# Kernel tuning notes

Measured on AMD Instinct MI355X. Metric: run time of the kernel, lower is better.

The kernel has to match this reference:

```python
import jax, jax.numpy as jnp
import numpy as np

EPS = 1e-5


def cheb_conv(x, edge, W, b):
    # x: [B, N, C], edge: [2, E], W: [3, C, F], b: [F]
    # PyG ChebConv, K=3, normalized Laplacian, lambda_max=2 -> L_hat = -D^-1/2 A D^-1/2
    row, col = edge[0], edge[1]
    N = x.shape[1]
    deg = jnp.zeros((N,), x.dtype).at[row].add(1.0)
    dis = jnp.where(deg > 0, 1.0 / jnp.sqrt(jnp.maximum(deg, 1.0)), 0.0)
    we = (-dis[row] * dis[col])[None, :, None]  # [1, E, 1]
    prop = lambda z: jnp.zeros_like(z).at[:, row].add(z[:, col] * we)
    Tx0 = x
    Tx1 = prop(Tx0)
    Tx2 = 2.0 * prop(Tx1) - Tx0
    out = (jnp.einsum('bnc,cf->bnf', Tx0, W[0])
           + jnp.einsum('bnc,cf->bnf', Tx1, W[1])
           + jnp.einsum('bnc,cf->bnf', Tx2, W[2]))
    return out + b


def lbr(x, W, b, g, be):
    # Linear -> BatchNorm1d (batch stats) -> ReLU (dropout prob = 0)
    h = x @ W + b
    h = (h - h.mean(0)) / jnp.sqrt(h.var(0) + EPS) * g + be
    return jax.nn.relu(h)


def setup_inputs() -> dict:
    key = jax.random.key(0)
    ks = jax.random.split(key, 32)
    B, H = 32, 32
    Ns = [16384, 4096, 1024, 128]
    Es = [131072, 32768, 8192, 1024]
    F = Ns[3] * H  # 4096 flattened dim
    L = 128
    d = {}
    d['x'] = jax.random.normal(ks[0], (B, Ns[0], 3), jnp.float32)
    for i in range(4):
        d[f'e{i}'] = jax.random.randint(ks[1 + i], (2, Es[i]), 0, Ns[i])
    for i in range(3):
        d[f'l{i}'] = jnp.sort(jax.random.randint(ks[5 + i], (Ns[i + 1],), 0, Ns[i]))
    s = 0.1
    d['Wc1'] = jax.random.normal(ks[8], (3, 3, H), jnp.float32) * s
    d['b1'] = jnp.zeros((H,), jnp.float32)
    for i, nm in enumerate(['Wc2', 'Wc3', 'Wc4', 'Wc5']):
        d[nm] = jax.random.normal(ks[9 + i], (3, H, H), jnp.float32) * s
        d['b' + str(i + 2)] = jnp.zeros((H,), jnp.float32)
    sf = 1.0 / np.sqrt(F).astype(np.float32)
    for i, nm in enumerate(['W6', 'W7', 'W8']):
        d[nm] = jax.random.normal(ks[13 + i], (F, F), jnp.float32) * sf
        d['b' + str(i + 6)] = jnp.zeros((F,), jnp.float32)
        d['g' + str(i + 6)] = jnp.ones((F,), jnp.float32)
        d['be' + str(i + 6)] = jnp.zeros((F,), jnp.float32)
    d['W9'] = jax.random.normal(ks[16], (F, L), jnp.float32) * sf
    d['b9'] = jnp.zeros((L,), jnp.float32)
    return d


def reference(x, Wc1, b1, Wc2, b2, Wc3, b3, Wc4, b4, Wc5, b5,
              W6, b6, g6, be6, W7, b7, g7, be7, W8, b8, g8, be8, W9, b9,
              e0, e1, e2, e3, l0, l1, l2):
    x = cheb_conv(x, e0, Wc1, b1)                       # level 0
    x = jnp.tanh(cheb_conv(x[:, l0], e1, Wc2, b2))      # CTP: pool -> Cheb -> tanh
    x = jnp.tanh(cheb_conv(x[:, l1], e2, Wc3, b3))
    x = jnp.tanh(cheb_conv(x[:, l2], e3, Wc4, b4))
    x = cheb_conv(x, e3, Wc5, b5)                       # level 3, [B, N3, H]
    x = x.reshape(x.shape[0], -1)                       # [B, N3*H]
    x = lbr(lbr(lbr(x, W6, b6, g6, be6), W7, b7, g7, be7), W8, b8, g8, be8)
    mu = x @ W9 + b9
    mu = (mu - mu.mean(0)) / jnp.sqrt(mu.var(0) + EPS)  # BatchNorm1d affine=False
    return mu
```

## Files before the change

### kernel.cpp

```cpp
#include <hip/hip_runtime.h>
#include <hip/hip_bf16.h>

#define BB 32
#define HD 32
#define N0 16384
#define C0 3
#define E0v 131072
#define N1 4096
#define E1v 32768
#define N2 1024
#define E2v 8192
#define N3 128
#define E3v 1024
#define FDIM 4096
#define LDIM 128
#define NT (N0 + N1 + N2 + N3)
#define ET (E0v + E1v + E2v + E3v)
#define EPSBN 1e-5f
#define KC 64

__global__ void k_count(const int* __restrict__ e0, const int* __restrict__ e1,
                        const int* __restrict__ e2, const int* __restrict__ e3,
                        int* __restrict__ deg) {
    int e = blockIdx.x * 256 + threadIdx.x;
    if (e >= ET) return;
    const int* p; int idx, nb;
    if (e < E0v)                     { p = e0; idx = e; nb = 0; }
    else if (e < E0v + E1v)          { p = e1; idx = e - E0v; nb = N0; }
    else if (e < E0v + E1v + E2v)    { p = e2; idx = e - E0v - E1v; nb = N0 + N1; }
    else                             { p = e3; idx = e - E0v - E1v - E2v; nb = N0 + N1 + N2; }
    atomicAdd(&deg[nb + p[idx]], 1);
}

__global__ void __launch_bounds__(1024) k_scan(const int* __restrict__ deg,
                                               int* __restrict__ offs, int* __restrict__ cur) {
    __shared__ int ss[1024];
    int t = threadIdx.x, base = t * 22;
    int loc[22]; int s = 0;
#pragma unroll
    for (int i = 0; i < 22; i++) {
        int idx = base + i;
        int v = (idx < NT) ? deg[idx] : 0;
        loc[i] = s; s += v;
    }
    ss[t] = s;
    __syncthreads();
    int run = s;
    for (int o = 1; o < 1024; o <<= 1) {
        int y = (t >= o) ? ss[t - o] : 0;
        __syncthreads();
        run += y; ss[t] = run;
        __syncthreads();
    }
    int excl = run - s;
#pragma unroll
    for (int i = 0; i < 22; i++) {
        int idx = base + i;
        if (idx < NT) { int v = excl + loc[i]; offs[idx] = v; cur[idx] = v; }
    }
    if (t == 0) offs[NT] = ET;
}

__global__ void k_scatter(const int* __restrict__ e0, const int* __restrict__ e1,
                          const int* __restrict__ e2, const int* __restrict__ e3,
                          const int* __restrict__ deg, int* __restrict__ cur,
                          int* __restrict__ ccol, float* __restrict__ cw) {
    int e = blockIdx.x * 256 + threadIdx.x;
    if (e >= ET) return;
    const int* p; int idx, nb, El;
    if (e < E0v)                  { p = e0; idx = e; nb = 0; El = E0v; }
    else if (e < E0v + E1v)       { p = e1; idx = e - E0v; nb = N0; El = E1v; }
    else if (e < E0v + E1v + E2v) { p = e2; idx = e - E0v - E1v; nb = N0 + N1; El = E2v; }
    else                          { p = e3; idx = e - E0v - E1v - E2v; nb = N0 + N1 + N2; El = E3v; }
    int r = p[idx], c = p[El + idx];
    int pos = atomicAdd(&cur[nb + r], 1);
    int dr = deg[nb + r], dc = deg[nb + c];
    float w = 0.f;
    if (dr > 0 && dc > 0)
        w = -(1.f / sqrtf((float)dr)) * (1.f / sqrtf((float)dc));
    ccol[pos] = c;
    cw[pos] = w;
}

__global__ void k_transpose(const float* __restrict__ x, float* __restrict__ xt) {
    __shared__ float t0[32][33], t1[32][33], t2[32][33];
    int tx = threadIdx.x, ty = threadIdx.y;
    int n0 = blockIdx.x * 32;
#pragma unroll
    for (int i = 0; i < 4; i++) {
        int b = ty * 4 + i;
        size_t base = ((size_t)b * N0 + n0 + tx) * 3;
        t0[tx][b] = x[base];
        t1[tx][b] = x[base + 1];
        t2[tx][b] = x[base + 2];
    }
    __syncthreads();
#pragma unroll
    for (int i = 0; i < 4; i++) {
        int nl = ty * 4 + i;
        size_t o = (size_t)(n0 + nl) * 96 + tx * 3;
        xt[o]     = t0[nl][tx];
        xt[o + 1] = t1[nl][tx];
        xt[o + 2] = t2[nl][tx];
    }
}

__global__ void k_prop0(const float* __restrict__ xt, float* __restrict__ T1t,
                        const int* __restrict__ offs, const int* __restrict__ ccol,
                        const float* __restrict__ cw) {
    int idx = blockIdx.x * 256 + threadIdx.x;
    int n = (unsigned)idx / 96u;
    int q = idx - n * 96;
    int s = offs[n], e = offs[n + 1];
    float acc = 0.f;
    for (int k = s; k < e; k++)
        acc += cw[k] * xt[(size_t)ccol[k] * 96 + q];
    T1t[idx] = acc;
}

__global__ void k_comb0(const float* __restrict__ xt, const float* __restrict__ T1t,
                        const int* __restrict__ offs, const int* __restrict__ ccol,
                        const float* __restrict__ cw, const int* __restrict__ pool,
                        const float* __restrict__ W, const float* __restrict__ bias,
                        float* __restrict__ Yout) {
    __shared__ float s0[96], s1[96], s2[96], sw[288], sb[32];
    int t = threadIdx.x;
    int j = blockIdx.x;
    int n = pool[j];
    size_t nb = (size_t)n * 96;
    s0[t] = xt[nb + t];
    s1[t] = T1t[nb + t];
    if (t < 32) { s0[64 + t] = xt[nb + 64 + t]; s1[64 + t] = T1t[nb + 64 + t]; }
    {
        int s = offs[n], e = offs[n + 1];
        float a0 = 0.f, a1 = 0.f;
        for (int k = s; k < e; k++) {
            const float* bp = T1t + (size_t)ccol[k] * 96;
            float w = cw[k];
            a0 += w * bp[t];
            if (t < 32) a1 += w * bp[64 + t];
        }
        s2[t] = a0;
        if (t < 32) s2[64 + t] = a1;
    }
    for (int i = t; i < 288; i += 64) sw[i] = W[i];
    if (t < 32) sb[t] = bias[t];
    __syncthreads();

    int f0 = (t & 7) * 4;
    int b0 = (t >> 3) * 4;
    float acc[4][4];
#pragma unroll
    for (int bi = 0; bi < 4; bi++)
#pragma unroll
        for (int fi = 0; fi < 4; fi++) acc[bi][fi] = sb[f0 + fi];
#pragma unroll
    for (int c = 0; c < 3; c++) {
        float4 w0 = *(float4*)&sw[(0 * 3 + c) * 32 + f0];
        float4 w1 = *(float4*)&sw[(1 * 3 + c) * 32 + f0];
        float4 w2 = *(float4*)&sw[(2 * 3 + c) * 32 + f0];
#pragma unroll
        for (int bi = 0; bi < 4; bi++) {
            int b = b0 + bi;
            float x0 = s0[b * 3 + c], x1 = s1[b * 3 + c];
            float x2 = 2.f * s2[b * 3 + c] - x0;
            acc[bi][0] += x0 * w0.x + x1 * w1.x + x2 * w2.x;
            acc[bi][1] += x0 * w0.y + x1 * w1.y + x2 * w2.y;
            acc[bi][2] += x0 * w0.z + x1 * w1.z + x2 * w2.z;
            acc[bi][3] += x0 * w0.w + x1 * w1.w + x2 * w2.w;
        }
    }
#pragma unroll
    for (int bi = 0; bi < 4; bi++) {
        float4 v = { acc[bi][0], acc[bi][1], acc[bi][2], acc[bi][3] };
        *(float4*)&Yout[(size_t)j * 1024 + (b0 + bi) * 32 + f0] = v;
    }
}

__global__ void k_propC(const float* __restrict__ Yin, float* __restrict__ T1,
                        const int* __restrict__ offs, const int* __restrict__ ccol,
                        const float* __restrict__ cw) {
    int idx = blockIdx.x * 256 + threadIdx.x;
    int n = idx >> 10;
    int q = idx & 1023;
    int s = offs[n], e = offs[n + 1];
    float acc = 0.f;
    for (int k = s; k < e; k++)
        acc += cw[k] * Yin[((size_t)ccol[k] << 10) + q];
    T1[idx] = acc;
}

__global__ void k_combC(const float* __restrict__ Yin, const float* __restrict__ T1,
                        const int* __restrict__ offs, const int* __restrict__ ccol,
                        const float* __restrict__ cw, const int* __restrict__ pool,
                        const float* __restrict__ W, const float* __restrict__ bias,
                        float* __restrict__ Yout, int doTanh, int bMajor) {
    __shared__ float s0[32 * 33], s1[32 * 33], s2[32 * 33], sw[3072], sb[32];
    int t = threadIdx.x;
    int j = blockIdx.x;
    int n = pool ? pool[j] : j;
    size_t nb = (size_t)n << 10;
#pragma unroll
    for (int i = 0; i < 16; i++) {
        int q = t + i * 64;
        int li = (q >> 5) * 33 + (q & 31);
        s0[li] = Yin[nb + q];
        s1[li] = T1[nb + q];
    }
    {
        int s = offs[n], e = offs[n + 1];
        float ga[16];
#pragma unroll
        for (int i = 0; i < 16; i++) ga[i] = 0.f;
        for (int k = s; k < e; k++) {
            const float* bp = T1 + ((size_t)ccol[k] << 10);
            float w = cw[k];
#pragma unroll
            for (int i = 0; i < 16; i++) ga[i] += w * bp[t + i * 64];
        }
#pragma unroll
        for (int i = 0; i < 16; i++) {
            int q = t + i * 64;
            s2[(q >> 5) * 33 + (q & 31)] = ga[i];
        }
    }
    for (int i = t; i < 768; i += 64) ((float4*)sw)[i] = ((const float4*)W)[i];
    if (t < 32) sb[t] = bias[t];
    __syncthreads();

    int f0 = (t & 7) * 4;
    int b0 = (t >> 3) * 4;
    float acc[4][4];
#pragma unroll
    for (int bi = 0; bi < 4; bi++)
#pragma unroll
        for (int fi = 0; fi < 4; fi++) acc[bi][fi] = sb[f0 + fi];
    for (int c = 0; c < 32; c++) {
        float4 w0 = *(float4*)&sw[c * 32 + f0];
        float4 w1 = *(float4*)&sw[1024 + c * 32 + f0];
        float4 w2 = *(float4*)&sw[2048 + c * 32 + f0];
#pragma unroll
        for (int bi = 0; bi < 4; bi++) {
            int li = (b0 + bi) * 33 + c;
            float x0 = s0[li], x1 = s1[li];
            float x2 = 2.f * s2[li] - x0;
            acc[bi][0] += x0 * w0.x + x1 * w1.x + x2 * w2.x;
            acc[bi][1] += x0 * w0.y + x1 * w1.y + x2 * w2.y;
            acc[bi][2] += x0 * w0.z + x1 * w1.z + x2 * w2.z;
            acc[bi][3] += x0 * w0.w + x1 * w1.w + x2 * w2.w;
        }
    }
    if (doTanh) {
#pragma unroll
        for (int bi = 0; bi < 4; bi++)
#pragma unroll
            for (int fi = 0; fi < 4; fi++) acc[bi][fi] = tanhf(acc[bi][fi]);
    }
#pragma unroll
    for (int bi = 0; bi < 4; bi++) {
        float4 v = { acc[bi][0], acc[bi][1], acc[bi][2], acc[bi][3] };
        if (bMajor)
            *(float4*)&Yout[(size_t)(b0 + bi) * FDIM + j * 32 + f0] = v;
        else
            *(float4*)&Yout[((size_t)j << 10) + (b0 + bi) * 32 + f0] = v;
    }
}

__global__ void __launch_bounds__(256, 2) k_gemm(const float* __restrict__ Z,
                                                 const float* __restrict__ W,
                                                 float* __restrict__ Hp) {
    int t = threadIdx.x; int bx = blockIdx.x; int kc = blockIdx.y; int kb = kc * 64;
    __shared__ float zs[32][64];
    for (int i = t; i < 512; i += 256) {
        int fl = i * 4; int b = fl >> 6; int k = fl & 63;
        *(float4*)&zs[b][k] = *(const float4*)&Z[(size_t)b * 4096 + kb + k];
    }
    __syncthreads();
    int ft = t & 63, bt = t >> 6;
    int f0 = bx * 256 + ft * 4;
    int b0 = bt * 8;
    const float* Wp = W + (size_t)kb * 4096 + f0;
    float acc[8][4];
#pragma unroll
    for (int bi = 0; bi < 8; bi++)
#pragma unroll
        for (int fi = 0; fi < 4; fi++) acc[bi][fi] = 0.f;
    for (int k4 = 0; k4 < 16; k4++) {
        float4 w[4];
#pragma unroll
        for (int j = 0; j < 4; j++)
            w[j] = *(const float4*)&Wp[(size_t)(k4 * 4 + j) * 4096];
        float4 z[8];
#pragma unroll
        for (int bi = 0; bi < 8; bi++)
            z[bi] = *(const float4*)&zs[b0 + bi][k4 * 4];
#pragma unroll
        for (int bi = 0; bi < 8; bi++) {
            acc[bi][0] += z[bi].x * w[0].x + z[bi].y * w[1].x + z[bi].z * w[2].x + z[bi].w * w[3].x;
            acc[bi][1] += z[bi].x * w[0].y + z[bi].y * w[1].y + z[bi].z * w[2].y + z[bi].w * w[3].y;
            acc[bi][2] += z[bi].x * w[0].z + z[bi].y * w[1].z + z[bi].z * w[2].z + z[bi].w * w[3].z;
            acc[bi][3] += z[bi].x * w[0].w + z[bi].y * w[1].w + z[bi].z * w[2].w + z[bi].w * w[3].w;
        }
    }
    float* o = Hp + (size_t)kc * 32 * 4096;
#pragma unroll
    for (int bi = 0; bi < 8; bi++) {
        float4 v = { acc[bi][0], acc[bi][1], acc[bi][2], acc[bi][3] };
        *(float4*)&o[(size_t)(b0 + bi) * 4096 + f0] = v;
    }
}

__global__ void k_bnrelu(const float* __restrict__ Hp, const float* __restrict__ g,
                         const float* __restrict__ be, float* __restrict__ Zo) {
    __shared__ float sA[8][33], sB[8][33], sm[32], si[32];
    int t = threadIdx.x; int fq = t & 31; int bq = t >> 5;
    int f = blockIdx.x * 32 + fq;
    float v[4];
#pragma unroll
    for (int i = 0; i < 4; i++) v[i] = 0.f;
    for (int p = 0; p < KC; p++) {
        const float* hp = Hp + (size_t)p * 32 * 4096;
#pragma unroll
        for (int i = 0; i < 4; i++) v[i] += hp[(size_t)(bq * 4 + i) * 4096 + f];
    }
    float a = 0.f, q = 0.f;
#pragma unroll
    for (int i = 0; i < 4; i++) { a += v[i]; q += v[i] * v[i]; }
    sA[bq][fq] = a; sB[bq][fq] = q;
    __syncthreads();
    if (t < 32) {
        float m = 0.f, qq = 0.f;
#pragma unroll
        for (int i = 0; i < 8; i++) { m += sA[i][t]; qq += sB[i][t]; }
        m *= (1.f / 32.f);
        qq = qq * (1.f / 32.f) - m * m;
        sm[t] = m; si[t] = rsqrtf(fmaxf(qq, 0.f) + EPSBN);
    }
    __syncthreads();
    float m = sm[fq], inv = si[fq], gg = g[f], bb = be[f];
#pragma unroll
    for (int i = 0; i < 4; i++) {
        float o = (v[i] - m) * inv * gg + bb;
        Zo[(size_t)(bq * 4 + i) * 4096 + f] = fmaxf(o, 0.f);
    }
}

__global__ void __launch_bounds__(128, 2) k_gemm9(const float* __restrict__ Z,
                                                  const float* __restrict__ W9,
                                                  float* __restrict__ Mp) {
    int t = threadIdx.x; int kc = blockIdx.x; int kb = kc * 64;
    __shared__ float zs[32][64];
    for (int i = t; i < 512; i += 128) {
        int fl = i * 4; int b = fl >> 6; int k = fl & 63;
        *(float4*)&zs[b][k] = *(const float4*)&Z[(size_t)b * 4096 + kb + k];
    }
    __syncthreads();
    int ft = t & 31, bt = t >> 5;
    int f0 = ft * 4;
    int b0 = bt * 8;
    const float* Wp = W9 + (size_t)kb * 128 + f0;
    float acc[8][4];
#pragma unroll
    for (int bi = 0; bi < 8; bi++)
#pragma unroll
        for (int fi = 0; fi < 4; fi++) acc[bi][fi] = 0.f;
    for (int k4 = 0; k4 < 16; k4++) {
        float4 w[4];
#pragma unroll
        for (int j = 0; j < 4; j++)
            w[j] = *(const float4*)&Wp[(size_t)(k4 * 4 + j) * 128];
        float4 z[8];
#pragma unroll
        for (int bi = 0; bi < 8; bi++)
            z[bi] = *(const float4*)&zs[b0 + bi][k4 * 4];
#pragma unroll
        for (int bi = 0; bi < 8; bi++) {
            acc[bi][0] += z[bi].x * w[0].x + z[bi].y * w[1].x + z[bi].z * w[2].x + z[bi].w * w[3].x;
            acc[bi][1] += z[bi].x * w[0].y + z[bi].y * w[1].y + z[bi].z * w[2].y + z[bi].w * w[3].y;
            acc[bi][2] += z[bi].x * w[0].z + z[bi].y * w[1].z + z[bi].z * w[2].z + z[bi].w * w[3].z;
            acc[bi][3] += z[bi].x * w[0].w + z[bi].y * w[1].w + z[bi].z * w[2].w + z[bi].w * w[3].w;
        }
    }
    float* o = Mp + (size_t)kc * 32 * 128;
#pragma unroll
    for (int bi = 0; bi < 8; bi++) {
        float4 v = { acc[bi][0], acc[bi][1], acc[bi][2], acc[bi][3] };
        *(float4*)&o[(b0 + bi) * 128 + f0] = v;
    }
}

__global__ void k_red9(const float* __restrict__ Mp, float* __restrict__ Mu) {
    int idx = blockIdx.x * 256 + threadIdx.x;
    if (idx >= 4096) return;
    float a = 0.f;
    for (int p = 0; p < KC; p++) a += Mp[(size_t)p * 4096 + idx];
    Mu[idx] = a;
}

__global__ void k_bnfinal(const float* __restrict__ Mu, float* __restrict__ out) {
    int f = threadIdx.x;
    float v[32], s = 0.f;
#pragma unroll
    for (int b = 0; b < 32; b++) { v[b] = Mu[b * 128 + f]; s += v[b]; }
    float m = s * (1.f / 32.f), q = 0.f;
#pragma unroll
    for (int b = 0; b < 32; b++) { float d = v[b] - m; q += d * d; }
    float inv = rsqrtf(q * (1.f / 32.f) + EPSBN);
#pragma unroll
    for (int b = 0; b < 32; b++) out[b * 128 + f] = (v[b] - m) * inv;
}

extern "C" void kernel_launch(void* const* d_in, const int* in_sizes, int n_in,
                              void* d_out, int out_size, void* d_ws, size_t ws_size,
                              hipStream_t stream) {
    const float* x  = (const float*)d_in[0];
    const int* e0 = (const int*)d_in[1];
    const int* e1 = (const int*)d_in[2];
    const int* e2 = (const int*)d_in[3];
    const int* e3 = (const int*)d_in[4];
    const int* l0 = (const int*)d_in[5];
    const int* l1 = (const int*)d_in[6];
    const int* l2 = (const int*)d_in[7];
    const float* Wc1 = (const float*)d_in[8];
    const float* b1  = (const float*)d_in[9];
    const float* Wc2 = (const float*)d_in[10];
    const float* b2  = (const float*)d_in[11];
    const float* Wc3 = (const float*)d_in[12];
    const float* b3  = (const float*)d_in[13];
    const float* Wc4 = (const float*)d_in[14];
    const float* b4  = (const float*)d_in[15];
    const float* Wc5 = (const float*)d_in[16];
    const float* b5  = (const float*)d_in[17];
    const float* W6  = (const float*)d_in[18];
    const float* g6  = (const float*)d_in[20];
    const float* be6 = (const float*)d_in[21];
    const float* W7  = (const float*)d_in[22];
    const float* g7  = (const float*)d_in[24];
    const float* be7 = (const float*)d_in[25];
    const float* W8  = (const float*)d_in[26];
    const float* g8  = (const float*)d_in[28];
    const float* be8 = (const float*)d_in[29];
    const float* W9  = (const float*)d_in[30];
    float* out = (float*)d_out;

    char* p = (char*)d_ws;
    size_t o = 0;
    auto carve = [&](size_t bytes) {
        void* r = (void*)(p + o);
        o += (bytes + 255) & ~(size_t)255;
        return r;
    };
    float* xt  = (float*)carve((size_t)N0 * 96 * 4);
    float* T1t = (float*)carve((size_t)N0 * 96 * 4);
    float* Y1  = (float*)carve((size_t)N1 * 1024 * 4);
    float* T1c = (float*)carve((size_t)N1 * 1024 * 4);
    float* Y2  = (float*)carve((size_t)N2 * 1024 * 4);
    float* Y3  = (float*)carve((size_t)N3 * 1024 * 4);
    float* Y4  = (float*)carve((size_t)N3 * 1024 * 4);
    float* Zb0 = (float*)carve((size_t)BB * FDIM * 4);
    float* Zb1 = (float*)carve((size_t)BB * FDIM * 4);
    float* Mp  = (float*)carve((size_t)KC * BB * LDIM * 4);
    float* Mu  = (float*)carve((size_t)BB * LDIM * 4);
    int* deg  = (int*)carve(NT * sizeof(int));
    int* offs = (int*)carve((NT + 1) * sizeof(int));
    int* cur  = (int*)carve(NT * sizeof(int));
    int* ccol = (int*)carve(ET * sizeof(int));
    float* cw = (float*)carve(ET * sizeof(float));
    float* Hp = xt;
    (void)ws_size;

    hipMemsetAsync(deg, 0, NT * sizeof(int), stream);
    k_count<<<(ET + 255) / 256, 256, 0, stream>>>(e0, e1, e2, e3, deg);
    k_scan<<<1, 1024, 0, stream>>>(deg, offs, cur);
    k_scatter<<<(ET + 255) / 256, 256, 0, stream>>>(e0, e1, e2, e3, deg, cur, ccol, cw);

    const int* off0 = offs;
    const int* off1 = offs + N0;
    const int* off2 = offs + N0 + N1;
    const int* off3 = offs + N0 + N1 + N2;

    k_transpose<<<N0 / 32, dim3(32, 8), 0, stream>>>(x, xt);

    k_prop0<<<(N0 * 96) / 256, 256, 0, stream>>>(xt, T1t, off0, ccol, cw);
    k_comb0<<<N1, 64, 0, stream>>>(xt, T1t, off0, ccol, cw, l0, Wc1, b1, Y1);
    k_propC<<<(N1 * 1024) / 256, 256, 0, stream>>>(Y1, T1c, off1, ccol, cw);
    k_combC<<<N2, 64, 0, stream>>>(Y1, T1c, off1, ccol, cw, l1, Wc2, b2, Y2, 1, 0);
    k_propC<<<(N2 * 1024) / 256, 256, 0, stream>>>(Y2, T1c, off2, ccol, cw);
    k_combC<<<N3, 64, 0, stream>>>(Y2, T1c, off2, ccol, cw, l2, Wc3, b3, Y3, 1, 0);
    k_propC<<<(N3 * 1024) / 256, 256, 0, stream>>>(Y3, T1c, off3, ccol, cw);
    k_combC<<<N3, 64, 0, stream>>>(Y3, T1c, off3, ccol, cw, nullptr, Wc4, b4, Y4, 1, 0);
    k_propC<<<(N3 * 1024) / 256, 256, 0, stream>>>(Y4, T1c, off3, ccol, cw);
    k_combC<<<N3, 64, 0, stream>>>(Y4, T1c, off3, ccol, cw, nullptr, Wc5, b5, Zb0, 0, 1);

    const float* Ws[3]  = { W6, W7, W8 };
    const float* gs[3]  = { g6, g7, g8 };
    const float* bes[3] = { be6, be7, be8 };
    float* zin = Zb0; float* zout = Zb1;
    for (int l = 0; l < 3; l++) {
        k_gemm<<<dim3(16, KC), 256, 0, stream>>>(zin, Ws[l], Hp);
        k_bnrelu<<<128, 256, 0, stream>>>(Hp, gs[l], bes[l], zout);
        float* tmp = zin; zin = zout; zout = tmp;
    }
    k_gemm9<<<KC, 128, 0, stream>>>(zin, W9, Mp);
    k_red9<<<16, 256, 0, stream>>>(Mp, Mu);
    k_bnfinal<<<1, 128, 0, stream>>>(Mu, out);
    (void)out_size; (void)n_in; (void)in_sizes;
}
```

Before: 533.6 us.

## Pack CSR edges, vectorize gathers with float4, and reduce GEMM split-K partials

Stores each CSR edge's column and weight together as an int2 so the gathers issue one load per edge. The propagation and combine kernels now gather float4 vectors, and propC runs one block per node. The dense GEMM's split-K factor drops from 64 to 16, with each block looping over four 64-wide K sub-chunks, which shrinks the partial-sum buffer written and then re-reduced by the BN kernel. The risk is fewer GEMM blocks, which may underfill the GPU while streaming the weights.

Measured after the change: 553.1 us. +3.7%, slower.

```diff
diff --git a/kernel.cpp b/kernel.cpp
--- a/kernel.cpp
+++ b/kernel.cpp
@@ -17,7 +17,8 @@
 #define NT (N0 + N1 + N2 + N3)
 #define ET (E0v + E1v + E2v + E3v)
 #define EPSBN 1e-5f
-#define KC 64
+#define KC 16
+#define KC9 64
 
 __global__ void k_count(const int* __restrict__ e0, const int* __restrict__ e1,
                         const int* __restrict__ e2, const int* __restrict__ e3,
@@ -64,7 +65,7 @@
 __global__ void k_scatter(const int* __restrict__ e0, const int* __restrict__ e1,
                           const int* __restrict__ e2, const int* __restrict__ e3,
                           const int* __restrict__ deg, int* __restrict__ cur,
-                          int* __restrict__ ccol, float* __restrict__ cw) {
+                          int2* __restrict__ cpk) {
     int e = blockIdx.x * 256 + threadIdx.x;
     if (e >= ET) return;
     const int* p; int idx, nb, El;
@@ -78,8 +79,7 @@
     float w = 0.f;
     if (dr > 0 && dc > 0)
         w = -(1.f / sqrtf((float)dr)) * (1.f / sqrtf((float)dc));
-    ccol[pos] = c;
-    cw[pos] = w;
+    cpk[pos] = make_int2(c, __float_as_int(w));
 }
 
 __global__ void k_transpose(const float* __restrict__ x, float* __restrict__ xt) {
@@ -106,42 +106,44 @@
 }
 
 __global__ void k_prop0(const float* __restrict__ xt, float* __restrict__ T1t,
-                        const int* __restrict__ offs, const int* __restrict__ ccol,
-                        const float* __restrict__ cw) {
+                        const int* __restrict__ offs, const int2* __restrict__ cpk) {
     int idx = blockIdx.x * 256 + threadIdx.x;
-    int n = (unsigned)idx / 96u;
-    int q = idx - n * 96;
+    int n = (unsigned)idx / 24u;
+    int q = (idx - n * 24) * 4;
     int s = offs[n], e = offs[n + 1];
-    float acc = 0.f;
-    for (int k = s; k < e; k++)
-        acc += cw[k] * xt[(size_t)ccol[k] * 96 + q];
-    T1t[idx] = acc;
+    float4 acc = { 0.f, 0.f, 0.f, 0.f };
+    for (int k = s; k < e; k++) {
+        int2 ew = cpk[k];
+        float w = __int_as_float(ew.y);
+        float4 v = *(const float4*)&xt[(size_t)ew.x * 96 + q];
+        acc.x += w * v.x; acc.y += w * v.y; acc.z += w * v.z; acc.w += w * v.w;
+    }
+    *(float4*)&T1t[(size_t)n * 96 + q] = acc;
 }
 
 __global__ void k_comb0(const float* __restrict__ xt, const float* __restrict__ T1t,
-                        const int* __restrict__ offs, const int* __restrict__ ccol,
-                        const float* __restrict__ cw, const int* __restrict__ pool,
+                        const int* __restrict__ offs, const int2* __restrict__ cpk,
+                        const int* __restrict__ pool,
                         const float* __restrict__ W, const float* __restrict__ bias,
                         float* __restrict__ Yout) {
-    __shared__ float s0[96], s1[96], s2[96], sw[288], sb[32];
+    __shared__ __align__(16) float s0[96], s1[96], s2[96];
+    __shared__ float sw[288], sb[32];
     int t = threadIdx.x;
     int j = blockIdx.x;
     int n = pool[j];
     size_t nb = (size_t)n * 96;
-    s0[t] = xt[nb + t];
-    s1[t] = T1t[nb + t];
-    if (t < 32) { s0[64 + t] = xt[nb + 64 + t]; s1[64 + t] = T1t[nb + 64 + t]; }
-    {
+    if (t < 24) {
+        *(float4*)&s0[t * 4] = *(const float4*)&xt[nb + t * 4];
+        *(float4*)&s1[t * 4] = *(const float4*)&T1t[nb + t * 4];
         int s = offs[n], e = offs[n + 1];
-        float a0 = 0.f, a1 = 0.f;
+        float4 ga = { 0.f, 0.f, 0.f, 0.f };
         for (int k = s; k < e; k++) {
-            const float* bp = T1t + (size_t)ccol[k] * 96;
-            float w = cw[k];
-            a0 += w * bp[t];
-            if (t < 32) a1 += w * bp[64 + t];
-        }
-        s2[t] = a0;
-        if (t < 32) s2[64 + t] = a1;
+            int2 ew = cpk[k];
+            float w = __int_as_float(ew.y);
+            float4 v = *(const float4*)&T1t[(size_t)ew.x * 96 + t * 4];
+            ga.x += w * v.x; ga.y += w * v.y; ga.z += w * v.z; ga.w += w * v.w;
+        }
+        *(float4*)&s2[t * 4] = ga;
     }
     for (int i = t; i < 288; i += 64) sw[i] = W[i];
     if (t < 32) sb[t] = bias[t];
@@ -178,21 +180,23 @@
 }
 
 __global__ void k_propC(const float* __restrict__ Yin, float* __restrict__ T1,
-                        const int* __restrict__ offs, const int* __restrict__ ccol,
-                        const float* __restrict__ cw) {
-    int idx = blockIdx.x * 256 + threadIdx.x;
-    int n = idx >> 10;
-    int q = idx & 1023;
+                        const int* __restrict__ offs, const int2* __restrict__ cpk) {
+    int n = blockIdx.x;
+    int q = threadIdx.x * 4;
     int s = offs[n], e = offs[n + 1];
-    float acc = 0.f;
-    for (int k = s; k < e; k++)
-        acc += cw[k] * Yin[((size_t)ccol[k] << 10) + q];
-    T1[idx] = acc;
+    float4 acc = { 0.f, 0.f, 0.f, 0.f };
+    for (int k = s; k < e; k++) {
+        int2 ew = cpk[k];
+        float w = __int_as_float(ew.y);
+        float4 v = *(const float4*)&Yin[((size_t)ew.x << 10) + q];
+        acc.x += w * v.x; acc.y += w * v.y; acc.z += w * v.z; acc.w += w * v.w;
+    }
+    *(float4*)&T1[((size_t)n << 10) + q] = acc;
 }
 
 __global__ void k_combC(const float* __restrict__ Yin, const float* __restrict__ T1,
-                        const int* __restrict__ offs, const int* __restrict__ ccol,
-                        const float* __restrict__ cw, const int* __restrict__ pool,
+                        const int* __restrict__ offs, const int2* __restrict__ cpk,
+                        const int* __restrict__ pool,
                         const float* __restrict__ W, const float* __restrict__ bias,
                         float* __restrict__ Yout, int doTanh, int bMajor) {
     __shared__ float s0[32 * 33], s1[32 * 33], s2[32 * 33], sw[3072], sb[32];
@@ -201,27 +205,35 @@
     int n = pool ? pool[j] : j;
     size_t nb = (size_t)n << 10;
 #pragma unroll
-    for (int i = 0; i < 16; i++) {
-        int q = t + i * 64;
+    for (int i = 0; i < 4; i++) {
+        int q = t * 4 + i * 256;
+        float4 v0 = *(const float4*)&Yin[nb + q];
+        float4 v1 = *(const float4*)&T1[nb + q];
         int li = (q >> 5) * 33 + (q & 31);
-        s0[li] = Yin[nb + q];
-        s1[li] = T1[nb + q];
+        s0[li] = v0.x; s0[li + 1] = v0.y; s0[li + 2] = v0.z; s0[li + 3] = v0.w;
+        s1[li] = v1.x; s1[li + 1] = v1.y; s1[li + 2] = v1.z; s1[li + 3] = v1.w;
     }
     {
         int s = offs[n], e = offs[n + 1];
-        float ga[16];
-#pragma unroll
-        for (int i = 0; i < 16; i++) ga[i] = 0.f;
+        float4 ga[4];
+#pragma unroll
+        for (int i = 0; i < 4; i++) ga[i] = make_float4(0.f, 0.f, 0.f, 0.f);
         for (int k = s; k < e; k++) {
-            const float* bp = T1 + ((size_t)ccol[k] << 10);
-            float w = cw[k];
-#pragma unroll
-            for (int i = 0; i < 16; i++) ga[i] += w * bp[t + i * 64];
-        }
-#pragma unroll
-        for (int i = 0; i < 16; i++) {
-            int q = t + i * 64;
-            s2[(q >> 5) * 33 + (q & 31)] = ga[i];
+            int2 ew = cpk[k];
+            float w = __int_as_float(ew.y);
+            const float* bp = T1 + ((size_t)ew.x << 10);
+#pragma unroll
+            for (int i = 0; i < 4; i++) {
+                float4 v = *(const float4*)&bp[t * 4 + i * 256];
+                ga[i].x += w * v.x; ga[i].y += w * v.y;
+                ga[i].z += w * v.z; ga[i].w += w * v.w;
+            }
+        }
+#pragma unroll
+        for (int i = 0; i < 4; i++) {
+            int q = t * 4 + i * 256;
+            int li = (q >> 5) * 33 + (q & 31);
+            s2[li] = ga[i].x; s2[li + 1] = ga[i].y; s2[li + 2] = ga[i].z; s2[li + 3] = ga[i].w;
         }
     }
     for (int i = t; i < 768; i += 64) ((float4*)sw)[i] = ((const float4*)W)[i];
@@ -269,37 +281,41 @@
 __global__ void __launch_bounds__(256, 2) k_gemm(const float* __restrict__ Z,
                                                  const float* __restrict__ W,
                                                  float* __restrict__ Hp) {
-    int t = threadIdx.x; int bx = blockIdx.x; int kc = blockIdx.y; int kb = kc * 64;
+    int t = threadIdx.x; int bx = blockIdx.x; int kc = blockIdx.y;
     __shared__ float zs[32][64];
-    for (int i = t; i < 512; i += 256) {
-        int fl = i * 4; int b = fl >> 6; int k = fl & 63;
-        *(float4*)&zs[b][k] = *(const float4*)&Z[(size_t)b * 4096 + kb + k];
-    }
-    __syncthreads();
     int ft = t & 63, bt = t >> 6;
     int f0 = bx * 256 + ft * 4;
     int b0 = bt * 8;
-    const float* Wp = W + (size_t)kb * 4096 + f0;
     float acc[8][4];
 #pragma unroll
     for (int bi = 0; bi < 8; bi++)
 #pragma unroll
         for (int fi = 0; fi < 4; fi++) acc[bi][fi] = 0.f;
-    for (int k4 = 0; k4 < 16; k4++) {
-        float4 w[4];
-#pragma unroll
-        for (int j = 0; j < 4; j++)
-            w[j] = *(const float4*)&Wp[(size_t)(k4 * 4 + j) * 4096];
-        float4 z[8];
-#pragma unroll
-        for (int bi = 0; bi < 8; bi++)
-            z[bi] = *(const float4*)&zs[b0 + bi][k4 * 4];
-#pragma unroll
-        for (int bi = 0; bi < 8; bi++) {
-            acc[bi][0] += z[bi].x * w[0].x + z[bi].y * w[1].x + z[bi].z * w[2].x + z[bi].w * w[3].x;
-            acc[bi][1] += z[bi].x * w[0].y + z[bi].y * w[1].y + z[bi].z * w[2].y + z[bi].w * w[3].y;
-            acc[bi][2] += z[bi].x * w[0].z + z[bi].y * w[1].z + z[bi].z * w[2].z + z[bi].w * w[3].z;
-            acc[bi][3] += z[bi].x * w[0].w + z[bi].y * w[1].w + z[bi].z * w[2].w + z[bi].w * w[3].w;
+    for (int sc = 0; sc < 4; sc++) {
+        int kb = kc * 256 + sc * 64;
+        __syncthreads();
+        for (int i = t; i < 512; i += 256) {
+            int fl = i * 4; int b = fl >> 6; int k = fl & 63;
+            *(float4*)&zs[b][k] = *(const float4*)&Z[(size_t)b * 4096 + kb + k];
+        }
+        __syncthreads();
+        const float* Wp = W + (size_t)kb * 4096 + f0;
+        for (int k4 = 0; k4 < 16; k4++) {
+            float4 w[4];
+#pragma unroll
+            for (int j = 0; j < 4; j++)
+                w[j] = *(const float4*)&Wp[(size_t)(k4 * 4 + j) * 4096];
+            float4 z[8];
+#pragma unroll
+            for (int bi = 0; bi < 8; bi++)
+                z[bi] = *(const float4*)&zs[b0 + bi][k4 * 4];
+#pragma unroll
+            for (int bi = 0; bi < 8; bi++) {
+                acc[bi][0] += z[bi].x * w[0].x + z[bi].y * w[1].x + z[bi].z * w[2].x + z[bi].w * w[3].x;
+                acc[bi][1] += z[bi].x * w[0].y + z[bi].y * w[1].y + z[bi].z * w[2].y + z[bi].w * w[3].y;
+                acc[bi][2] += z[bi].x * w[0].z + z[bi].y * w[1].z + z[bi].z * w[2].z + z[bi].w * w[3].z;
+                acc[bi][3] += z[bi].x * w[0].w + z[bi].y * w[1].w + z[bi].z * w[2].w + z[bi].w * w[3].w;
+            }
         }
     }
     float* o = Hp + (size_t)kc * 32 * 4096;
@@ -393,7 +409,7 @@
     int idx = blockIdx.x * 256 + threadIdx.x;
     if (idx >= 4096) return;
     float a = 0.f;
-    for (int p = 0; p < KC; p++) a += Mp[(size_t)p * 4096 + idx];
+    for (int p = 0; p < KC9; p++) a += Mp[(size_t)p * 4096 + idx];
     Mu[idx] = a;
 }
 
@@ -459,20 +475,19 @@
     float* Y4  = (float*)carve((size_t)N3 * 1024 * 4);
     float* Zb0 = (float*)carve((size_t)BB * FDIM * 4);
     float* Zb1 = (float*)carve((size_t)BB * FDIM * 4);
-    float* Mp  = (float*)carve((size_t)KC * BB * LDIM * 4);
+    float* Mp  = (float*)carve((size_t)KC9 * BB * LDIM * 4);
     float* Mu  = (float*)carve((size_t)BB * LDIM * 4);
     int* deg  = (int*)carve(NT * sizeof(int));
     int* offs = (int*)carve((NT + 1) * sizeof(int));
     int* cur  = (int*)carve(NT * sizeof(int));
-    int* ccol = (int*)carve(ET * sizeof(int));
-    float* cw = (float*)carve(ET * sizeof(float));
+    int2* cpk = (int2*)carve(ET * sizeof(int2));
     float* Hp = xt;
     (void)ws_size;
 
     hipMemsetAsync(deg, 0, NT * sizeof(int), stream);
     k_count<<<(ET + 255) / 256, 256, 0, stream>>>(e0, e1, e2, e3, deg);
     k_scan<<<1, 1024, 0, stream>>>(deg, offs, cur);
-    k_scatter<<<(ET + 255) / 256, 256, 0, stream>>>(e0, e1, e2, e3, deg, cur, ccol, cw);
+    k_scatter<<<(ET + 255) / 256, 256, 0, stream>>>(e0, e1, e2, e3, deg, cur, cpk);
 
     const int* off0 = offs;
     const int* off1 = offs + N0;
@@ -481,16 +496,16 @@
 
     k_transpose<<<N0 / 32, dim3(32, 8), 0, stream>>>(x, xt);
 
-    k_prop0<<<(N0 * 96) / 256, 256, 0, stream>>>(xt, T1t, off0, ccol, cw);
-    k_comb0<<<N1, 64, 0, stream>>>(xt, T1t, off0, ccol, cw, l0, Wc1, b1, Y1);
-    k_propC<<<(N1 * 1024) / 256, 256, 0, stream>>>(Y1, T1c, off1, ccol, cw);
-    k_combC<<<N2, 64, 0, stream>>>(Y1, T1c, off1, ccol, cw, l1, Wc2, b2, Y2, 1, 0);
-    k_propC<<<(N2 * 1024) / 256, 256, 0, stream>>>(Y2, T1c, off2, ccol, cw);
-    k_combC<<<N3, 64, 0, stream>>>(Y2, T1c, off2, ccol, cw, l2, Wc3, b3, Y3, 1, 0);
-    k_propC<<<(N3 * 1024) / 256, 256, 0, stream>>>(Y3, T1c, off3, ccol, cw);
-    k_combC<<<N3, 64, 0, stream>>>(Y3, T1c, off3, ccol, cw, nullptr, Wc4, b4, Y4, 1, 0);
-    k_propC<<<(N3 * 1024) / 256, 256, 0, stream>>>(Y4, T1c, off3, ccol, cw);
-    k_combC<<<N3, 64, 0, stream>>>(Y4, T1c, off3, ccol, cw, nullptr, Wc5, b5, Zb0, 0, 1);
+    k_prop0<<<(N0 * 24) / 256, 256, 0, stream>>>(xt, T1t, off0, cpk);
+    k_comb0<<<N1, 64, 0, stream>>>(xt, T1t, off0, cpk, l0, Wc1, b1, Y1);
+    k_propC<<<N1, 256, 0, stream>>>(Y1, T1c, off1, cpk);
+    k_combC<<<N2, 64, 0, stream>>>(Y1, T1c, off1, cpk, l1, Wc2, b2, Y2, 1, 0);
+    k_propC<<<N2, 256, 0, stream>>>(Y2, T1c, off2, cpk);
+    k_combC<<<N3, 64, 0, stream>>>(Y2, T1c, off2, cpk, l2, Wc3, b3, Y3, 1, 0);
+    k_propC<<<N3, 256, 0, stream>>>(Y3, T1c, off3, cpk);
+    k_combC<<<N3, 64, 0, stream>>>(Y3, T1c, off3, cpk, nullptr, Wc4, b4, Y4, 1, 0);
+    k_propC<<<N3, 256, 0, stream>>>(Y4, T1c, off3, cpk);
+    k_combC<<<N3, 64, 0, stream>>>(Y4, T1c, off3, cpk, nullptr, Wc5, b5, Zb0, 0, 1);
 
     const float* Ws[3]  = { W6, W7, W8 };
     const float* gs[3]  = { g6, g7, g8 };
@@ -501,7 +516,7 @@
         k_bnrelu<<<128, 256, 0, stream>>>(Hp, gs[l], bes[l], zout);
         float* tmp = zin; zin = zout; zout = tmp;
     }
-    k_gemm9<<<KC, 128, 0, stream>>>(zin, W9, Mp);
+    k_gemm9<<<KC9, 128, 0, stream>>>(zin, W9, Mp);
     k_red9<<<16, 256, 0, stream>>>(Mp, Mu);
     k_bnfinal<<<1, 128, 0, stream>>>(Mu, out);
     (void)out_size; (void)n_in; (void)in_sizes;
```
